# Kernel optimization log

Measured on AMD Instinct MI355X. Metric: run time of the kernel, lower is better.

Reference implementation:

```python
import jax, jax.numpy as jnp
import numpy as np

B, M, H, E = 1, 2048, 16, 128
D = H * E          # 2048, model dim
C = 4 * D          # 8192, FFN dim
F = E
G = D
J = D


def setup_inputs() -> dict:
    key = jax.random.key(0)
    k_in, k_wv, k_wk, k_wq, k_wz, k_ffa, k_ffb = jax.random.split(key, 7)
    scale = 0.01
    return {
        "I_in": jax.random.normal(k_in, (B, M, D), dtype=jnp.float32),
        "WV": jax.random.normal(k_wv, (H, E, D), dtype=jnp.float32) * scale,
        "WK": jax.random.normal(k_wk, (H, E, D), dtype=jnp.float32) * scale,
        "WQ": jax.random.normal(k_wq, (H, E, D), dtype=jnp.float32) * scale,
        "WZ": jax.random.normal(k_wz, (H, F, G), dtype=jnp.float32) * scale,
        "WFFA": jax.random.normal(k_ffa, (G, C), dtype=jnp.float32) * scale,
        "WFFB": jax.random.normal(k_ffb, (C, J), dtype=jnp.float32) * scale,
    }


def reference(I_in, WV, WK, WQ, WZ, WFFA, WFFB):
    # QKV projections: [B,M,D] x [H,E,D] -> [B,M,H,E]
    V = jnp.einsum('bmd,hed->bmhe', I_in, WV)
    K = jnp.einsum('bmd,hed->bmhe', I_in, WK)
    Q = jnp.einsum('bmd,hed->bmhe', I_in, WQ)
    # Attention scores [B,M,P,H]; NOTE: no 1/sqrt(E) scaling in the original.
    QK = jnp.einsum('bmhe,bphe->bmph', Q, K)
    # Softmax over keys (p axis = 2), matching torch.softmax(QK, dim=2)
    QK_softmax = jax.nn.softmax(QK, axis=2)
    # Attention output [B,M,H,E]
    AV = jnp.einsum('bmph,bphe->bmhe', QK_softmax, V)
    # Output projection [B,M,G]
    Z = jnp.einsum('bmhf,hfg->bmg', AV, WZ)
    # FFN (no nonlinearity in the original workload)
    FFA = jnp.einsum('bmg,gc->bmc', Z, WFFA)
    FFB = jnp.einsum('bmc,cj->bmj', FFA, WFFB)
    return FFB
```

## Files before the change

### kernel.cpp

```cpp
#include <hip/hip_runtime.h>
#include <hip/hip_bf16.h>
#include <math.h>


typedef __bf16 bf16_t;
typedef __bf16 bf16x8 __attribute__((ext_vector_type(8)));
typedef float  f32x4  __attribute__((ext_vector_type(4)));

#define AS1 __attribute__((address_space(1)))
#define AS3 __attribute__((address_space(3)))

__device__ __forceinline__ void load16_lds(const bf16_t* g, bf16_t* l) {
    __builtin_amdgcn_global_load_lds((AS1 void*)g, (AS3 void*)l, 16, 0, 0);
}

__device__ __forceinline__ void stageA_half(const bf16_t* __restrict__ Ab, int lda,
                                            int k0, int h, bf16_t* slot,
                                            int w, int lane)
{
    #pragma unroll
    for (int j = 0; j < 2; ++j) {
        const int prw = j * 64 + w * 8;
        const int p   = prw + (lane >> 3);
        const int lr  = (p >> 6) * 128 + h * 64 + (p & 63);
        const int lc  = (lane & 7) ^ (p & 7);
        load16_lds(Ab + (long long)lr * lda + k0 + lc * 8, slot + prw * 64);
    }
}
__device__ __forceinline__ void stageB_half(const bf16_t* __restrict__ Bb, int ldb,
                                            int k0, int h, bf16_t* slot,
                                            int w, int lane)
{
    #pragma unroll
    for (int j = 0; j < 2; ++j) {
        const int prw = j * 64 + w * 8;
        const int p   = prw + (lane >> 3);
        const int lr  = (p >> 5) * 64 + h * 32 + (p & 31);
        const int lc  = (lane & 7) ^ (p & 7);
        load16_lds(Bb + (long long)lr * ldb + k0 + lc * 8, slot + prw * 64);
    }
}

#define LOADAF(DST, SL)                                                        \
  _Pragma("unroll") for (int ks = 0; ks < 2; ++ks)                             \
  _Pragma("unroll") for (int mi = 0; mi < 4; ++mi)                             \
      DST[ks][mi] = *(const bf16x8*)&(SL)[(wm * 64 + mi * 16 + c15) * 64 +     \
                      (((ks * 4 + q4) ^ (c15 & 7)) * 8)];

#define LOADBV(DST, SL)                                                        \
  _Pragma("unroll") for (int ks = 0; ks < 2; ++ks)                             \
  _Pragma("unroll") for (int nj = 0; nj < 2; ++nj)                             \
      DST[ks][nj] = *(const bf16x8*)&(SL)[(wn * 32 + nj * 16 + c15) * 64 +     \
                      (((ks * 4 + q4) ^ (c15 & 7)) * 8)];

#define MFMA8(R0, C0)                                                          \
  _Pragma("unroll") for (int ks = 0; ks < 2; ++ks)                             \
  _Pragma("unroll") for (int mi = 0; mi < 4; ++mi)                             \
  _Pragma("unroll") for (int nj = 0; nj < 2; ++nj)                             \
      acc[(R0) + mi][(C0) + nj] = __builtin_amdgcn_mfma_f32_16x16x32_bf16(     \
          af[ks][mi], bv[ks][nj], acc[(R0) + mi][(C0) + nj], 0, 0, 0);

#define VMW(N)  asm volatile("s_waitcnt vmcnt(" #N ")" ::: "memory")
#define LGKM0() asm volatile("s_waitcnt lgkmcnt(0)" ::: "memory")
#define BAR()   __builtin_amdgcn_s_barrier()

#define PHASE8(RDS, STGS, GATE, R0, C0)                                        \
  RDS;                                                                         \
  STGS;                                                                        \
  GATE;                                                                        \
  __builtin_amdgcn_s_barrier();                                                \
  asm volatile("s_waitcnt lgkmcnt(0)" ::: "memory");                           \
  __builtin_amdgcn_sched_barrier(0);                                           \
  __builtin_amdgcn_s_setprio(1);                                               \
  MFMA8(R0, C0);                                                               \
  __builtin_amdgcn_s_setprio(0);                                               \
  __builtin_amdgcn_s_barrier();

template<typename TOUT>
__global__ __launch_bounds__(512, 2)
void gemm256p_bt(const bf16_t* __restrict__ A, const bf16_t* __restrict__ B,
                 TOUT* __restrict__ Cc, int Kdim,
                 int lda, int ldb, int ldc,
                 long long ab, long long bb, long long cb,
                 int ct_z, bf16_t* __restrict__ ctc, int ldct)
{
    __shared__ __attribute__((aligned(16))) bf16_t As4[4][128 * 64];
    __shared__ __attribute__((aligned(16))) bf16_t Bs4[4][128 * 64];

    const int z = blockIdx.z;
    A  += (long long)z * ab;
    B  += (long long)z * bb;
    Cc += (long long)z * cb;

    const int bm = blockIdx.y * 256;
    const int bn = blockIdx.x * 256;
    const int t = threadIdx.x, lane = t & 63, w = t >> 6;
    const int wm = w >> 2, wn = w & 3;
    const int q4 = lane >> 4, c15 = lane & 15;

    const bf16_t* Ab = A + (long long)bm * lda;
    const bf16_t* Bb = B + (long long)bn * ldb;

    f32x4  acc[8][4] = {};
    bf16x8 af[2][4];
    bf16x8 bv[2][2];

    stageB_half(Bb, ldb, 0,  0, Bs4[0], w, lane);
    stageA_half(Ab, lda, 0,  1, As4[1], w, lane);
    stageA_half(Ab, lda, 0,  0, As4[0], w, lane);
    stageB_half(Bb, ldb, 0,  1, Bs4[1], w, lane);
    stageB_half(Bb, ldb, 64, 0, Bs4[2], w, lane);
    stageA_half(Ab, lda, 64, 1, As4[3], w, lane);
    VMW(4);
    BAR();

    const int NT = Kdim >> 6;
    const int kcap = (NT - 1) << 6;

    for (int i = 0; i < NT / 2; ++i) {
        const int u  = 2 * i;
        const int k1 = (u + 1) << 6;
        int k2 = (u + 2) << 6; if (k2 > kcap) k2 = kcap;
        int k3 = (u + 3) << 6; if (k3 > kcap) k3 = kcap;
        PHASE8( LOADAF(af, As4[0]); LOADBV(bv, Bs4[0]),
                stageA_half(Ab, lda, k1, 0, As4[2], w, lane), ((void)0), 0, 0)
        PHASE8( LOADAF(af, As4[1]),
                stageB_half(Bb, ldb, k1, 1, Bs4[3], w, lane), ((void)0), 4, 0)
        PHASE8( LOADBV(bv, Bs4[1]),
                stageB_half(Bb, ldb, k2, 0, Bs4[0], w, lane), ((void)0), 4, 2)
        PHASE8( LOADAF(af, As4[0]),
                stageA_half(Ab, lda, k2, 1, As4[1], w, lane), VMW(4), 0, 2)
        PHASE8( LOADAF(af, As4[2]); LOADBV(bv, Bs4[2]),
                stageA_half(Ab, lda, k2, 0, As4[0], w, lane), ((void)0), 0, 0)
        PHASE8( LOADAF(af, As4[3]),
                stageB_half(Bb, ldb, k2, 1, Bs4[1], w, lane), ((void)0), 4, 0)
        PHASE8( LOADBV(bv, Bs4[3]),
                stageB_half(Bb, ldb, k3, 0, Bs4[2], w, lane), ((void)0), 4, 2)
        PHASE8( LOADAF(af, As4[2]),
                stageA_half(Ab, lda, k3, 1, As4[3], w, lane), VMW(4), 0, 2)
    }
    VMW(0);

    const int rb = q4 * 4;
    if (z == ct_z) {
        #pragma unroll
        for (int mi = 0; mi < 8; ++mi) {
            const long long mb = bm + wm * 128 + mi * 16 + rb;
            #pragma unroll
            for (int nj = 0; nj < 4; ++nj) {
                const long long n = bn + wn * 64 + nj * 16 + c15;
                union { bf16_t b[4]; unsigned long long u; } o;
                #pragma unroll
                for (int r = 0; r < 4; ++r) o.b[r] = (bf16_t)acc[mi][nj][r];
                *(unsigned long long*)(ctc + n * ldct + mb) = o.u;
            }
        }
    } else {
        #pragma unroll
        for (int mi = 0; mi < 8; ++mi) {
            #pragma unroll
            for (int r = 0; r < 4; ++r) {
                const long long m = bm + wm * 128 + mi * 16 + rb + r;
                TOUT* crow = Cc + m * ldc + bn + wn * 64 + c15;
                #pragma unroll
                for (int nj = 0; nj < 4; ++nj)
                    crow[nj * 16] = (TOUT)acc[mi][nj][r];
            }
        }
    }
}

template<typename TOUT, bool ATOMIC>
__global__ __launch_bounds__(256)
void gemm_bt(const bf16_t* __restrict__ A, const bf16_t* __restrict__ B,
             TOUT* __restrict__ Cc, int Mdim, int Ndim, int Kdim,
             int lda, int ldb, int ldc,
             long long ab, long long bb, long long cb,
             int ct_z, bf16_t* __restrict__ ctc, int ldct)
{
    __shared__ bf16_t Ash[128 * 32];
    __shared__ bf16_t Bsh[128 * 32];

    const int z = blockIdx.z;
    A  += (long long)z * ab;
    B  += (long long)z * bb;
    Cc += (long long)z * cb;

    const int bm = blockIdx.y * 128;
    const int bn = blockIdx.x * 128;
    const int t  = threadIdx.x;
    const int lane = t & 63;
    const int w    = t >> 6;

    const int wm = (w & 1) * 64;
    const int wn = (w >> 1) * 64;

    const int sub = lane >> 2;
    const int seg = lane & 3;

    const bf16_t* Ag0 = A + (long long)(bm + w * 32 + sub) * lda + seg * 8;
    const bf16_t* Ag1 = Ag0 + 16LL * lda;
    const bf16_t* Bg0 = B + (long long)(bn + w * 32 + sub) * ldb + seg * 8;
    const bf16_t* Bg1 = Bg0 + 16LL * ldb;

    bf16_t* Al0 = &Ash[(w * 2 + 0) * 512];
    bf16_t* Al1 = &Ash[(w * 2 + 1) * 512];
    bf16_t* Bl0 = &Bsh[(w * 2 + 0) * 512];
    bf16_t* Bl1 = &Bsh[(w * 2 + 1) * 512];

    const int col  = lane & 15;
    const int koff = (lane >> 4) * 8;

    f32x4 acc[4][4] = {};

    for (int k0 = 0; k0 < Kdim; k0 += 32) {
        load16_lds(Ag0 + k0, Al0);
        load16_lds(Ag1 + k0, Al1);
        load16_lds(Bg0 + k0, Bl0);
        load16_lds(Bg1 + k0, Bl1);
        __syncthreads();

        bf16x8 afr[4], bfr[4];
        #pragma unroll
        for (int mi = 0; mi < 4; ++mi)
            afr[mi] = *(const bf16x8*)&Ash[(wm + mi * 16 + col) * 32 + koff];
        #pragma unroll
        for (int nj = 0; nj < 4; ++nj)
            bfr[nj] = *(const bf16x8*)&Bsh[(wn + nj * 16 + col) * 32 + koff];
        #pragma unroll
        for (int mi = 0; mi < 4; ++mi)
            #pragma unroll
            for (int nj = 0; nj < 4; ++nj)
                acc[mi][nj] = __builtin_amdgcn_mfma_f32_16x16x32_bf16(
                    afr[mi], bfr[nj], acc[mi][nj], 0, 0, 0);
        __syncthreads();
    }

    const int rbase = (lane >> 4) * 4;
    if (z == ct_z) {
        #pragma unroll
        for (int mi = 0; mi < 4; ++mi) {
            const long long mb = bm + wm + mi * 16 + rbase;
            #pragma unroll
            for (int nj = 0; nj < 4; ++nj) {
                const long long n = bn + wn + nj * 16 + col;
                union { bf16_t b[4]; unsigned long long u; } o;
                #pragma unroll
                for (int r = 0; r < 4; ++r) o.b[r] = (bf16_t)acc[mi][nj][r];
                *(unsigned long long*)(ctc + n * ldct + mb) = o.u;
            }
        }
    } else {
        #pragma unroll
        for (int mi = 0; mi < 4; ++mi) {
            #pragma unroll
            for (int r = 0; r < 4; ++r) {
                long long m = bm + wm + mi * 16 + rbase + r;
                TOUT* crow = Cc + m * ldc + bn + wn + col;
                #pragma unroll
                for (int nj = 0; nj < 4; ++nj) {
                    if constexpr (ATOMIC)
                        atomicAdd(&crow[nj * 16], (float)acc[mi][nj][r]);
                    else
                        crow[nj * 16] = (TOUT)acc[mi][nj][r];
                }
            }
        }
    }
}

__global__ __launch_bounds__(256, 2)
void flash_attn(const bf16_t* __restrict__ Q, const bf16_t* __restrict__ K,
                const bf16_t* __restrict__ VT, bf16_t* __restrict__ O,
                int M, int D)
{
    __shared__ bf16_t Kt[2][64 * 128];
    __shared__ bf16_t Vt[2][128 * 64];
    __shared__ bf16_t Pl[4 * 16 * 88];

    const int t = threadIdx.x, lane = t & 63, w = t >> 6;
    const int q4 = lane >> 4;
    const int c  = lane & 15;
    const int bm = blockIdx.x * 64;
    const int hE = blockIdx.y * 128;

    bf16x8 af_q[4];
    {
        const bf16_t* qrow = Q + (long long)(bm + w * 16 + c) * D + hE + q4 * 8;
        #pragma unroll
        for (int ks = 0; ks < 4; ++ks)
            af_q[ks] = *(const bf16x8*)(qrow + ks * 32);
    }

    f32x4 acc_o[8] = {};
    float m_i[4] = {-INFINITY, -INFINITY, -INFINITY, -INFINITY};
    float l_i[4] = {0.f, 0.f, 0.f, 0.f};

    bf16_t* Pw = &Pl[w * 16 * 88];

    const int NT = M >> 6;

    #define FA_STAGE(P0, B)                                                    \
      _Pragma("unroll")                                                        \
      for (int j = 0; j < 4; ++j) {                                            \
          int krow = w * 16 + j * 4;                                           \
          load16_lds(K + (long long)((P0) + krow + q4) * D + hE +              \
                         ((c ^ (j * 4 + q4)) * 8),                             \
                     &Kt[B][krow * 128]);                                      \
          int vrow = w * 32 + j * 8;                                           \
          load16_lds(VT + (long long)(hE + vrow + (lane >> 3)) * M + (P0) +    \
                         (((lane & 7) ^ (lane >> 3)) * 8),                     \
                     &Vt[B][vrow * 64]);                                       \
      }

    FA_STAGE(0, 0)

    for (int ti = 0; ti < NT; ++ti) {
        const int cur = ti & 1;
        const int pn = (ti + 1 < NT) ? (ti + 1) * 64 : ti * 64;
        FA_STAGE(pn, cur ^ 1)
        VMW(8);
        BAR();

        f32x4 acc_s[4] = {};
        __builtin_amdgcn_s_setprio(1);
        #pragma unroll
        for (int ks = 0; ks < 4; ++ks) {
            #pragma unroll
            for (int nj = 0; nj < 4; ++nj) {
                int row = nj * 16 + c;
                bf16x8 bk = *(const bf16x8*)&Kt[cur][row * 128 + (((ks * 4 + q4) ^ c) * 8)];
                acc_s[nj] = __builtin_amdgcn_mfma_f32_16x16x32_bf16(
                    af_q[ks], bk, acc_s[nj], 0, 0, 0);
            }
        }
        __builtin_amdgcn_s_setprio(0);

        float mt[4], alpha[4], rs[4];
        #pragma unroll
        for (int r = 0; r < 4; ++r) {
            float v = fmaxf(fmaxf(acc_s[0][r], acc_s[1][r]),
                            fmaxf(acc_s[2][r], acc_s[3][r]));
            #pragma unroll
            for (int off = 1; off < 16; off <<= 1)
                v = fmaxf(v, __shfl_xor(v, off));
            mt[r] = v;
        }
        #pragma unroll
        for (int r = 0; r < 4; ++r) {
            float mn = fmaxf(m_i[r], mt[r]);
            alpha[r] = __expf(m_i[r] - mn);
            m_i[r] = mn;
            rs[r] = 0.f;
        }
        #pragma unroll
        for (int nj = 0; nj < 4; ++nj)
            #pragma unroll
            for (int r = 0; r < 4; ++r) {
                float p = __expf(acc_s[nj][r] - m_i[r]);
                rs[r] += p;
                Pw[(q4 * 4 + r) * 88 + nj * 16 + c] = (bf16_t)p;
            }
        #pragma unroll
        for (int r = 0; r < 4; ++r) {
            float v = rs[r];
            #pragma unroll
            for (int off = 1; off < 16; off <<= 1)
                v += __shfl_xor(v, off);
            l_i[r] = alpha[r] * l_i[r] + v;
        }
        #pragma unroll
        for (int nj = 0; nj < 8; ++nj)
            #pragma unroll
            for (int r = 0; r < 4; ++r)
                acc_o[nj][r] *= alpha[r];

        LGKM0();
        __builtin_amdgcn_sched_barrier(0);

        __builtin_amdgcn_s_setprio(1);
        #pragma unroll
        for (int ks = 0; ks < 2; ++ks) {
            bf16x8 ap = *(const bf16x8*)&Pw[c * 88 + ks * 32 + q4 * 8];
            #pragma unroll
            for (int nj = 0; nj < 8; ++nj) {
                int row = nj * 16 + c;
                bf16x8 bvv = *(const bf16x8*)&Vt[cur][row * 64 + (((ks * 4 + q4) ^ (c & 7)) * 8)];
                acc_o[nj] = __builtin_amdgcn_mfma_f32_16x16x32_bf16(
                    ap, bvv, acc_o[nj], 0, 0, 0);
            }
        }
        __builtin_amdgcn_s_setprio(0);
        BAR();
    }
    VMW(0);

    float inv[4];
    #pragma unroll
    for (int r = 0; r < 4; ++r) inv[r] = 1.0f / l_i[r];
    #pragma unroll
    for (int nj = 0; nj < 8; ++nj)
        #pragma unroll
        for (int r = 0; r < 4; ++r)
            O[(long long)(bm + w * 16 + q4 * 4 + r) * D + hE + nj * 16 + c] =
                (bf16_t)(acc_o[nj][r] * inv[r]);
    #undef FA_STAGE
}

__global__ __launch_bounds__(256)
void cast4_bf16(const float* __restrict__ s0, const float* __restrict__ s1,
                const float* __restrict__ s2, const float* __restrict__ s3,
                bf16_t* __restrict__ d0, long long seg, long long n)
{
    const float* src = (blockIdx.y == 0) ? s0 : (blockIdx.y == 1) ? s1
                     : (blockIdx.y == 2) ? s2 : s3;
    bf16_t* dst = d0 + (long long)blockIdx.y * seg;
    long long i = ((long long)blockIdx.x * 256 + threadIdx.x) * 4;
    if (i >= n) return;
    float4 v = *(const float4*)(src + i);
    union { bf16_t b[4]; unsigned long long u; } o;
    o.b[0] = (bf16_t)v.x; o.b[1] = (bf16_t)v.y;
    o.b[2] = (bf16_t)v.z; o.b[3] = (bf16_t)v.w;
    *(unsigned long long*)(dst + i) = o.u;
}

__global__ __launch_bounds__(256)
void transpose_to_bf16(const float* __restrict__ in, bf16_t* __restrict__ out,
                       int rows, int cols)
{
    __shared__ bf16_t tile[32][33];
    const int r0 = blockIdx.y * 32, c0 = blockIdx.x * 32;
    const int tx = threadIdx.x & 31, ty = threadIdx.x >> 5;
    #pragma unroll
    for (int i = 0; i < 4; ++i) {
        int r = ty + i * 8;
        tile[r][tx] = (bf16_t)in[(long long)(r0 + r) * cols + c0 + tx];
    }
    __syncthreads();
    #pragma unroll
    for (int i = 0; i < 4; ++i) {
        int r = ty + i * 8;
        out[(long long)(c0 + r) * rows + r0 + tx] = tile[tx][r];
    }
}

__global__ __launch_bounds__(256)
void reduce4_f32(const float* __restrict__ p, float* __restrict__ out,
                 long long n)
{
    long long i = ((long long)blockIdx.x * 256 + threadIdx.x) * 4;
    if (i >= n) return;
    float4 a = *(const float4*)(p + i);
    float4 b = *(const float4*)(p + n + i);
    float4 c = *(const float4*)(p + 2 * n + i);
    float4 d = *(const float4*)(p + 3 * n + i);
    float4 o;
    o.x = a.x + b.x + c.x + d.x;
    o.y = a.y + b.y + c.y + d.y;
    o.z = a.z + b.z + c.z + d.z;
    o.w = a.w + b.w + c.w + d.w;
    *(float4*)(out + i) = o;
}

extern "C" void kernel_launch(void* const* d_in, const int* in_sizes, int n_in,
                              void* d_out, int out_size, void* d_ws, size_t ws_size,
                              hipStream_t stream)
{
    const float* I    = (const float*)d_in[0];
    const float* WV   = (const float*)d_in[1];
    const float* WK   = (const float*)d_in[2];
    const float* WQ   = (const float*)d_in[3];
    const float* WZ   = (const float*)d_in[4];
    const float* WFFA = (const float*)d_in[5];
    const float* WFFB = (const float*)d_in[6];
    float* out = (float*)d_out;

    const int M = 2048, D = 2048, C = 8192;
    const long long MD = (long long)M * D;
    const size_t MiB = 1024 * 1024;

    char* base = (char*)d_ws;
    bf16_t* bI     = (bf16_t*)(base + 0 * MiB);
    bf16_t* bWQ    = (bf16_t*)(base + 8 * MiB);
    bf16_t* bWK    = (bf16_t*)(base + 16 * MiB);
    bf16_t* bWV    = (bf16_t*)(base + 24 * MiB);
    bf16_t* bQ     = (bf16_t*)(base + 32 * MiB);
    bf16_t* bK     = (bf16_t*)(base + 40 * MiB);
    bf16_t* bVT    = (bf16_t*)(base + 48 * MiB);
    bf16_t* bAV    = (bf16_t*)(base + 56 * MiB);
    bf16_t* bZ     = (bf16_t*)(base + 64 * MiB);
    bf16_t* bWZT   = (bf16_t*)(base + 72 * MiB);
    bf16_t* bWFFAT = (bf16_t*)(base + 80 * MiB);
    bf16_t* bWFFBT = (bf16_t*)(base + 112 * MiB);
    bf16_t* bFFA   = (bf16_t*)(base + 0 * MiB);
    float*  pF     = (float*)(base + 32 * MiB);

    const dim3 blk(256);
    const dim3 blk512(512);

    cast4_bf16<<<dim3(MD / 1024, 4), blk, 0, stream>>>(I, WQ, WK, WV, bI, MD, MD);
    transpose_to_bf16<<<dim3(D / 32, D / 32), blk, 0, stream>>>(WZ,   bWZT,   D, D);
    transpose_to_bf16<<<dim3(C / 32, D / 32), blk, 0, stream>>>(WFFA, bWFFAT, D, C);
    transpose_to_bf16<<<dim3(D / 32, C / 32), blk, 0, stream>>>(WFFB, bWFFBT, C, D);

    gemm256p_bt<bf16_t><<<dim3(8, 8, 3), blk512, 0, stream>>>(
        bI, bWQ, bQ, D, D, D, D, 0, MD, MD, 2, bVT, M);

    flash_attn<<<dim3(M / 64, 16), blk, 0, stream>>>(bQ, bK, bVT, bAV, M, D);

    gemm_bt<bf16_t, false><<<dim3(16, 16, 1), blk, 0, stream>>>(
        bAV, bWZT, bZ, M, D, D, D, D, D, 0, 0, 0, -1, nullptr, 0);

    gemm256p_bt<bf16_t><<<dim3(32, 8, 1), blk512, 0, stream>>>(
        bZ, bWFFAT, bFFA, D, D, D, C, 0, 0, 0, -1, nullptr, 0);

    gemm256p_bt<float><<<dim3(8, 8, 4), blk512, 0, stream>>>(
        bFFA, bWFFBT, pF, 2048, C, C, D, 2048, 2048, MD, -1, nullptr, 0);

    reduce4_f32<<<dim3((int)(MD / 1024)), blk, 0, stream>>>(pF, out, MD);
}
```

Baseline: 599.4 us.

## Use split-K 256 GEMM for WZ projection, lazy softmax rescale, DPP reductions

The output projection moves from the 128-tile gemm_bt to the 256-tile gemm256p_bt with a 2-way split over K. Each half writes fp32 partials, and a new reduce2_bf16 kernel sums them and casts to bf16. This is meant to improve per-block reuse while keeping enough blocks in flight, at the cost of extra fp32 traffic and one more launch. In flash attention, the row max and sum reductions use DPP row shifts instead of shuffles. The running-max rescale of the accumulator is skipped when the new max stays within 8 of the old one, a lazy-rescale trick that trades a small overflow margin for fewer multiplies and exps.

```diff
diff --git a/kernel.cpp b/kernel.cpp
--- a/kernel.cpp
+++ b/kernel.cpp
@@ -12,6 +12,31 @@
 
 __device__ __forceinline__ void load16_lds(const bf16_t* g, bf16_t* l) {
     __builtin_amdgcn_global_load_lds((AS1 void*)g, (AS3 void*)l, 16, 0, 0);
+}
+
+__device__ __forceinline__ float rowmax16(float v) {
+    int t;
+    t = __builtin_amdgcn_mov_dpp(__float_as_int(v), 0x128, 0xf, 0xf, true);
+    v = fmaxf(v, __int_as_float(t));
+    t = __builtin_amdgcn_mov_dpp(__float_as_int(v), 0x124, 0xf, 0xf, true);
+    v = fmaxf(v, __int_as_float(t));
+    t = __builtin_amdgcn_mov_dpp(__float_as_int(v), 0x122, 0xf, 0xf, true);
+    v = fmaxf(v, __int_as_float(t));
+    t = __builtin_amdgcn_mov_dpp(__float_as_int(v), 0x121, 0xf, 0xf, true);
+    v = fmaxf(v, __int_as_float(t));
+    return v;
+}
+__device__ __forceinline__ float rowsum16(float v) {
+    int t;
+    t = __builtin_amdgcn_mov_dpp(__float_as_int(v), 0x128, 0xf, 0xf, true);
+    v += __int_as_float(t);
+    t = __builtin_amdgcn_mov_dpp(__float_as_int(v), 0x124, 0xf, 0xf, true);
+    v += __int_as_float(t);
+    t = __builtin_amdgcn_mov_dpp(__float_as_int(v), 0x122, 0xf, 0xf, true);
+    v += __int_as_float(t);
+    t = __builtin_amdgcn_mov_dpp(__float_as_int(v), 0x121, 0xf, 0xf, true);
+    v += __int_as_float(t);
+    return v;
 }
 
 __device__ __forceinline__ void stageA_half(const bf16_t* __restrict__ Ab, int lda,
@@ -170,105 +195,6 @@
     }
 }
 
-template<typename TOUT, bool ATOMIC>
-__global__ __launch_bounds__(256)
-void gemm_bt(const bf16_t* __restrict__ A, const bf16_t* __restrict__ B,
-             TOUT* __restrict__ Cc, int Mdim, int Ndim, int Kdim,
-             int lda, int ldb, int ldc,
-             long long ab, long long bb, long long cb,
-             int ct_z, bf16_t* __restrict__ ctc, int ldct)
-{
-    __shared__ bf16_t Ash[128 * 32];
-    __shared__ bf16_t Bsh[128 * 32];
-
-    const int z = blockIdx.z;
-    A  += (long long)z * ab;
-    B  += (long long)z * bb;
-    Cc += (long long)z * cb;
-
-    const int bm = blockIdx.y * 128;
-    const int bn = blockIdx.x * 128;
-    const int t  = threadIdx.x;
-    const int lane = t & 63;
-    const int w    = t >> 6;
-
-    const int wm = (w & 1) * 64;
-    const int wn = (w >> 1) * 64;
-
-    const int sub = lane >> 2;
-    const int seg = lane & 3;
-
-    const bf16_t* Ag0 = A + (long long)(bm + w * 32 + sub) * lda + seg * 8;
-    const bf16_t* Ag1 = Ag0 + 16LL * lda;
-    const bf16_t* Bg0 = B + (long long)(bn + w * 32 + sub) * ldb + seg * 8;
-    const bf16_t* Bg1 = Bg0 + 16LL * ldb;
-
-    bf16_t* Al0 = &Ash[(w * 2 + 0) * 512];
-    bf16_t* Al1 = &Ash[(w * 2 + 1) * 512];
-    bf16_t* Bl0 = &Bsh[(w * 2 + 0) * 512];
-    bf16_t* Bl1 = &Bsh[(w * 2 + 1) * 512];
-
-    const int col  = lane & 15;
-    const int koff = (lane >> 4) * 8;
-
-    f32x4 acc[4][4] = {};
-
-    for (int k0 = 0; k0 < Kdim; k0 += 32) {
-        load16_lds(Ag0 + k0, Al0);
-        load16_lds(Ag1 + k0, Al1);
-        load16_lds(Bg0 + k0, Bl0);
-        load16_lds(Bg1 + k0, Bl1);
-        __syncthreads();
-
-        bf16x8 afr[4], bfr[4];
-        #pragma unroll
-        for (int mi = 0; mi < 4; ++mi)
-            afr[mi] = *(const bf16x8*)&Ash[(wm + mi * 16 + col) * 32 + koff];
-        #pragma unroll
-        for (int nj = 0; nj < 4; ++nj)
-            bfr[nj] = *(const bf16x8*)&Bsh[(wn + nj * 16 + col) * 32 + koff];
-        #pragma unroll
-        for (int mi = 0; mi < 4; ++mi)
-            #pragma unroll
-            for (int nj = 0; nj < 4; ++nj)
-                acc[mi][nj] = __builtin_amdgcn_mfma_f32_16x16x32_bf16(
-                    afr[mi], bfr[nj], acc[mi][nj], 0, 0, 0);
-        __syncthreads();
-    }
-
-    const int rbase = (lane >> 4) * 4;
-    if (z == ct_z) {
-        #pragma unroll
-        for (int mi = 0; mi < 4; ++mi) {
-            const long long mb = bm + wm + mi * 16 + rbase;
-            #pragma unroll
-            for (int nj = 0; nj < 4; ++nj) {
-                const long long n = bn + wn + nj * 16 + col;
-                union { bf16_t b[4]; unsigned long long u; } o;
-                #pragma unroll
-                for (int r = 0; r < 4; ++r) o.b[r] = (bf16_t)acc[mi][nj][r];
-                *(unsigned long long*)(ctc + n * ldct + mb) = o.u;
-            }
-        }
-    } else {
-        #pragma unroll
-        for (int mi = 0; mi < 4; ++mi) {
-            #pragma unroll
-            for (int r = 0; r < 4; ++r) {
-                long long m = bm + wm + mi * 16 + rbase + r;
-                TOUT* crow = Cc + m * ldc + bn + wn + col;
-                #pragma unroll
-                for (int nj = 0; nj < 4; ++nj) {
-                    if constexpr (ATOMIC)
-                        atomicAdd(&crow[nj * 16], (float)acc[mi][nj][r]);
-                    else
-                        crow[nj * 16] = (TOUT)acc[mi][nj][r];
-                }
-            }
-        }
-    }
-}
-
 __global__ __launch_bounds__(256, 2)
 void flash_attn(const bf16_t* __restrict__ Q, const bf16_t* __restrict__ K,
                 const bf16_t* __restrict__ VT, bf16_t* __restrict__ O,
@@ -336,44 +262,53 @@
         }
         __builtin_amdgcn_s_setprio(0);
 
-        float mt[4], alpha[4], rs[4];
+        float mt[4], rs[4];
         #pragma unroll
         for (int r = 0; r < 4; ++r) {
-            float v = fmaxf(fmaxf(acc_s[0][r], acc_s[1][r]),
-                            fmaxf(acc_s[2][r], acc_s[3][r]));
-            #pragma unroll
-            for (int off = 1; off < 16; off <<= 1)
-                v = fmaxf(v, __shfl_xor(v, off));
-            mt[r] = v;
-        }
-        #pragma unroll
-        for (int r = 0; r < 4; ++r) {
-            float mn = fmaxf(m_i[r], mt[r]);
-            alpha[r] = __expf(m_i[r] - mn);
-            m_i[r] = mn;
+            mt[r] = rowmax16(fmaxf(fmaxf(acc_s[0][r], acc_s[1][r]),
+                                   fmaxf(acc_s[2][r], acc_s[3][r])));
             rs[r] = 0.f;
         }
-        #pragma unroll
-        for (int nj = 0; nj < 4; ++nj)
+        bool ok = true;
+        #pragma unroll
+        for (int r = 0; r < 4; ++r) ok = ok && (mt[r] <= m_i[r] + 8.0f);
+        if (__all(ok)) {
+            #pragma unroll
+            for (int nj = 0; nj < 4; ++nj)
+                #pragma unroll
+                for (int r = 0; r < 4; ++r) {
+                    float p = __expf(acc_s[nj][r] - m_i[r]);
+                    rs[r] += p;
+                    Pw[(q4 * 4 + r) * 88 + nj * 16 + c] = (bf16_t)p;
+                }
+            #pragma unroll
+            for (int r = 0; r < 4; ++r)
+                l_i[r] += rowsum16(rs[r]);
+        } else {
+            float alpha[4];
             #pragma unroll
             for (int r = 0; r < 4; ++r) {
-                float p = __expf(acc_s[nj][r] - m_i[r]);
-                rs[r] += p;
-                Pw[(q4 * 4 + r) * 88 + nj * 16 + c] = (bf16_t)p;
+                float mn = fmaxf(m_i[r], mt[r]);
+                alpha[r] = __expf(m_i[r] - mn);
+                m_i[r] = mn;
             }
-        #pragma unroll
-        for (int r = 0; r < 4; ++r) {
-            float v = rs[r];
-            #pragma unroll
-            for (int off = 1; off < 16; off <<= 1)
-                v += __shfl_xor(v, off);
-            l_i[r] = alpha[r] * l_i[r] + v;
-        }
-        #pragma unroll
-        for (int nj = 0; nj < 8; ++nj)
+            #pragma unroll
+            for (int nj = 0; nj < 4; ++nj)
+                #pragma unroll
+                for (int r = 0; r < 4; ++r) {
+                    float p = __expf(acc_s[nj][r] - m_i[r]);
+                    rs[r] += p;
+                    Pw[(q4 * 4 + r) * 88 + nj * 16 + c] = (bf16_t)p;
+                }
             #pragma unroll
             for (int r = 0; r < 4; ++r)
-                acc_o[nj][r] *= alpha[r];
+                l_i[r] = alpha[r] * l_i[r] + rowsum16(rs[r]);
+            #pragma unroll
+            for (int nj = 0; nj < 8; ++nj)
+                #pragma unroll
+                for (int r = 0; r < 4; ++r)
+                    acc_o[nj][r] *= alpha[r];
+        }
 
         LGKM0();
         __builtin_amdgcn_sched_barrier(0);
@@ -460,6 +395,22 @@
     o.z = a.z + b.z + c.z + d.z;
     o.w = a.w + b.w + c.w + d.w;
     *(float4*)(out + i) = o;
+}
+
+__global__ __launch_bounds__(256)
+void reduce2_bf16(const float* __restrict__ p, bf16_t* __restrict__ out,
+                  long long n)
+{
+    long long i = ((long long)blockIdx.x * 256 + threadIdx.x) * 4;
+    if (i >= n) return;
+    float4 a = *(const float4*)(p + i);
+    float4 b = *(const float4*)(p + n + i);
+    union { bf16_t b[4]; unsigned long long u; } o;
+    o.b[0] = (bf16_t)(a.x + b.x);
+    o.b[1] = (bf16_t)(a.y + b.y);
+    o.b[2] = (bf16_t)(a.z + b.z);
+    o.b[3] = (bf16_t)(a.w + b.w);
+    *(unsigned long long*)(out + i) = o.u;
 }
 
 extern "C" void kernel_launch(void* const* d_in, const int* in_sizes, int n_in,
@@ -493,6 +444,7 @@
     bf16_t* bWFFAT = (bf16_t*)(base + 80 * MiB);
     bf16_t* bWFFBT = (bf16_t*)(base + 112 * MiB);
     bf16_t* bFFA   = (bf16_t*)(base + 0 * MiB);
+    float*  pZ     = (float*)(base + 0 * MiB);
     float*  pF     = (float*)(base + 32 * MiB);
 
     const dim3 blk(256);
@@ -508,8 +460,9 @@
 
     flash_attn<<<dim3(M / 64, 16), blk, 0, stream>>>(bQ, bK, bVT, bAV, M, D);
 
-    gemm_bt<bf16_t, false><<<dim3(16, 16, 1), blk, 0, stream>>>(
-        bAV, bWZT, bZ, M, D, D, D, D, D, 0, 0, 0, -1, nullptr, 0);
+    gemm256p_bt<float><<<dim3(8, 8, 2), blk512, 0, stream>>>(
+        bAV, bWZT, pZ, 1024, D, D, D, 1024, 1024, MD, -1, nullptr, 0);
+    reduce2_bf16<<<dim3((int)(MD / 1024)), blk, 0, stream>>>(pZ, bZ, MD);
 
     gemm256p_bt<bf16_t><<<dim3(32, 8, 1), blk512, 0, stream>>>(
         bZ, bWFFAT, bFFA, D, D, D, C, 0, 0, 0, -1, nullptr, 0);
```

After: 579.2 us. 1.03x faster.
